# Optimization experiments

Hardware: AMD Instinct MI355X
Metric: run time of the kernel (lower is better)

The kernel has to match this reference:

```python
import jax, jax.numpy as jnp
import numpy as np

F = 256          # number of features (input_size)
H1, H2, H3 = 128, 64, 32
OUT = 1          # output_size


def setup_inputs() -> dict:
    key = jax.random.key(0)
    ks = jax.random.split(key, 10)
    B = 8192
    # Kaiming-uniform-ish small init; exact init doesn't matter for a math reference.
    def w(k, shape, fan_in):
        lim = 1.0 / np.sqrt(fan_in)
        return jax.random.uniform(k, shape, jnp.float32, -lim, lim)
    return {
        "x": jax.random.normal(ks[0], (B, F), dtype=jnp.float32),
        "W1": w(ks[1], (F, H1), 1),          # Linear(1 -> H1) per feature
        "b1": w(ks[2], (F, H1), 1),
        "W2": w(ks[3], (F, H1, H2), H1),
        "b2": w(ks[4], (F, H2), H1),
        "W3": w(ks[5], (F, H2, H3), H2),
        "b3": w(ks[6], (F, H3), H2),
        "W4": w(ks[7], (F, H3, OUT), H3),
        "b4": w(ks[8], (F, OUT), H3),
        "bias": jnp.zeros((OUT,), dtype=jnp.float32),
    }


def reference(x, W1, b1, W2, b2, W3, b3, W4, b4, bias):
    # Fused form of the per-feature FeatureNN loop (eval mode: dropout = identity).
    # Layer 1: scalar input per feature -> H1
    h = jax.nn.relu(x[:, :, None] * W1[None, :, :] + b1[None, :, :])   # [B,F,H1]
    h = jax.nn.relu(jnp.einsum('bfh,fhk->bfk', h, W2) + b2[None])      # [B,F,H2]
    h = jax.nn.relu(jnp.einsum('bfh,fhk->bfk', h, W3) + b3[None])      # [B,F,H3]
    f_out = jnp.einsum('bfh,fhk->bfk', h, W4) + b4[None]               # [B,F,OUT]
    # torch.cat(dim=1).sum(dim=1, keepdim=True): sum over features and output cols
    out = jnp.sum(f_out, axis=(1, 2), keepdims=False)[:, None] + bias[None, :]
    return out  # [B, OUT] with OUT==1
```

## Files before the change

### kernel.cpp

```cpp
#include <hip/hip_runtime.h>
#include <math.h>


#define NF   256
#define NH1  128
#define NH2  64
#define NH3  32
#define NB   8192

#define NRANK 129
#define ROW4  17
#define ROWH  136
#define TBLDW 8960

typedef float    f32x16 __attribute__((ext_vector_type(16)));
typedef unsigned u32x4  __attribute__((ext_vector_type(4)));
typedef _Float16 h16x2  __attribute__((ext_vector_type(2)));
typedef _Float16 h16x8  __attribute__((ext_vector_type(8)));

__device__ __forceinline__ unsigned pkh2(unsigned sw, unsigned sb, h16x2 xh) {
    h16x2 r = __builtin_elementwise_fma(xh, __builtin_bit_cast(h16x2, sw),
                                            __builtin_bit_cast(h16x2, sb));
    h16x2 hz = {(_Float16)0.f, (_Float16)0.f};
    return __builtin_bit_cast(unsigned, __builtin_elementwise_max(r, hz));
}

__global__ __launch_bounds__(512) void build_tables(
    const float* __restrict__ W1, const float* __restrict__ b1,
    const float* __restrict__ W2, const float* __restrict__ b2,
    const float* __restrict__ bias, float* __restrict__ out,
    unsigned* __restrict__ ws)
{
    __shared__ u32x4 SP4[NRANK * ROW4];
    __shared__ float tkey[NH1];
    __shared__ int   tidx[NH1];
    __shared__ float w1s[NH1], b1s[NH1];
    __shared__ float Pbw[8][NH2], Pbb[8][NH2], Pdw[8][NH2], Pdb[8][NH2];

    const int f = blockIdx.x;
    const int t = (int)threadIdx.x;
    _Float16* SPh = (_Float16*)SP4;

    const int gid = f * 512 + t;
    if (gid < NB) out[gid] = bias[0];

    const float* __restrict__ gw2 = W2 + (size_t)f * NH1 * NH2;
    if (t < NH1) {
        float w  = W1[f * NH1 + t];
        float bb = b1[f * NH1 + t];
        w1s[t] = w; b1s[t] = bb;
        tkey[t] = (w != 0.0f) ? (-bb / w) : INFINITY;
        tidx[t] = t;
    }
    __syncthreads();

    for (int size = 2; size <= NH1; size <<= 1) {
        for (int stride = size >> 1; stride > 0; stride >>= 1) {
            if (t < 64) {
                int pos = ((t / stride) * (stride << 1)) + (t % stride);
                int par = pos + stride;
                bool up = ((pos & size) == 0);
                float a = tkey[pos], c = tkey[par];
                int  ia = tidx[pos], ic = tidx[par];
                if ((a > c) == up) {
                    tkey[pos] = c; tkey[par] = a;
                    tidx[pos] = ic; tidx[par] = ia;
                }
            }
            __syncthreads();
        }
    }

    {
        const int k = t & 63, c = t >> 6;
        float bw = 0.0f, bbp = 0.0f, dw = 0.0f, db = 0.0f;
        #pragma unroll 4
        for (int i = 0; i < 16; ++i) {
            int j = c * 16 + i;
            float w = w1s[j], bv = b1s[j], w2v = gw2[j * NH2 + k];
            if (w < 0.0f) { bw = fmaf(w, w2v, bw); bbp = fmaf(bv, w2v, bbp); }
            else if (w == 0.0f && bv > 0.0f) { bbp = fmaf(bv, w2v, bbp); }
            int jj = tidx[c * 16 + i];
            float ww = w1s[jj], bv2 = b1s[jj], w2x = gw2[jj * NH2 + k];
            float s = (ww > 0.0f) ? 1.0f : ((ww < 0.0f) ? -1.0f : 0.0f);
            dw = fmaf(s * ww,  w2x, dw);
            db = fmaf(s * bv2, w2x, db);
        }
        Pbw[c][k] = bw; Pbb[c][k] = bbp; Pdw[c][k] = dw; Pdb[c][k] = db;
    }
    __syncthreads();
    {
        const int k = t & 63, c = t >> 6;
        float accw = 0.0f;
        float accb = b2[f * NH2 + k];
        #pragma unroll
        for (int c2 = 0; c2 < 8; ++c2) { accw += Pbw[c2][k]; accb += Pbb[c2][k]; }
        for (int c2 = 0; c2 < c; ++c2) { accw += Pdw[c2][k]; accb += Pdb[c2][k]; }
        if (c == 0) {
            SPh[k]      = (_Float16)accw;
            SPh[64 + k] = (_Float16)accb;
        }
        #pragma unroll 4
        for (int i = 0; i < 16; ++i) {
            int r = c * 16 + i;
            int j = tidx[r];
            float w = w1s[j], bv = b1s[j], w2v = gw2[j * NH2 + k];
            float s = (w > 0.0f) ? 1.0f : ((w < 0.0f) ? -1.0f : 0.0f);
            accw = fmaf(s * w,  w2v, accw);
            accb = fmaf(s * bv, w2v, accb);
            SPh[(r + 1) * ROWH + k]      = (_Float16)accw;
            SPh[(r + 1) * ROWH + 64 + k] = (_Float16)accb;
        }
    }
    __syncthreads();

    unsigned* __restrict__ wsf = ws + (size_t)f * TBLDW;
    if (t < NH1) wsf[t] = __float_as_uint(tkey[t]);
    const u32x4* src = (const u32x4*)SP4;
    u32x4* dst = (u32x4*)(wsf + NH1);
    #pragma unroll 2
    for (int i = t; i < NRANK * ROW4; i += 512) dst[i] = src[i];
}

__global__ __launch_bounds__(512, 4) void nam_main(
    const float* __restrict__ x,
    const float* __restrict__ W3, const float* __restrict__ b3,
    const float* __restrict__ W4, const float* __restrict__ b4,
    const unsigned* __restrict__ ws,
    float* __restrict__ out)
{
    __shared__ u32x4 SP4[NRANK * ROW4];
    __shared__ float tkey[NH1];

    const int f  = blockIdx.x >> 2;
    const int qt = blockIdx.x & 3;
    const int t  = (int)threadIdx.x;

    const unsigned* __restrict__ wsf = ws + (size_t)f * TBLDW;
    if (t < NH1) tkey[t] = __uint_as_float(wsf[t]);
    {
        const u32x4* src = (const u32x4*)(wsf + NH1);
        #pragma unroll 2
        for (int i = t; i < NRANK * ROW4; i += 512) SP4[i] = src[i];
    }
    __syncthreads();

    const int lane = t & 63, wv = t >> 6;
    const int n = lane & 31, q2 = lane >> 5;

    const float* __restrict__ w3g = W3 + f * NH2 * NH3;
    h16x8 A0, A1, A2, A3;
    #pragma unroll
    for (int j = 0; j < 8; ++j) {
        int kk = q2 * 8 + j;
        A0[j] = (_Float16)w3g[kk * NH3 + n];
        A1[j] = (_Float16)w3g[(kk + 16) * NH3 + n];
        A2[j] = (_Float16)w3g[(kk + 32) * NH3 + n];
        A3[j] = (_Float16)w3g[(kk + 48) * NH3 + n];
    }
    float b3r[16], w4r[16];
    #pragma unroll
    for (int reg = 0; reg < 16; ++reg) {
        int row = (reg & 3) + 8 * (reg >> 2) + 4 * q2;
        b3r[reg] = b3[f * NH3 + row];
        w4r[reg] = W4[f * NH3 + row];
    }
    const float b4f = b4[f];
    const float t63 = tkey[63], t31 = tkey[31], t95 = tkey[95];
    const float t15 = tkey[15], t47 = tkey[47], t79 = tkey[79], t111 = tkey[111];

    #pragma unroll 1
    for (int round = 0; round < 8; ++round) {
        const int base = qt * 2048 + (round * 8 + wv) * 32;
        const float xv = x[(size_t)(base + n) * NF + f];

        int r = (t63 < xv) ? 64 : 0;
        {
            float l1 = (r & 64) ? t95 : t31;
            if (l1 < xv) r += 32;
            float m0 = (r & 64) ? t79  : t15;
            float m1 = (r & 64) ? t111 : t47;
            float l2 = (r & 32) ? m1 : m0;
            if (l2 < xv) r += 16;
        }
        #pragma unroll
        for (int s = 8; s > 0; s >>= 1)
            if (tkey[r + s - 1] < xv) r += s;

        const int ro = r * ROW4;
        u32x4 SW0 = SP4[ro + q2],      SW1 = SP4[ro + 2 + q2];
        u32x4 SW2 = SP4[ro + 4 + q2],  SW3 = SP4[ro + 6 + q2];
        u32x4 SB0 = SP4[ro + 8 + q2],  SB1 = SP4[ro + 10 + q2];
        u32x4 SB2 = SP4[ro + 12 + q2], SB3 = SP4[ro + 14 + q2];

        const h16x2 xh = {(_Float16)xv, (_Float16)xv};
        u32x4 d0, d1, d2, d3;
        d0.x = pkh2(SW0.x, SB0.x, xh); d0.y = pkh2(SW0.y, SB0.y, xh);
        d0.z = pkh2(SW0.z, SB0.z, xh); d0.w = pkh2(SW0.w, SB0.w, xh);
        d1.x = pkh2(SW1.x, SB1.x, xh); d1.y = pkh2(SW1.y, SB1.y, xh);
        d1.z = pkh2(SW1.z, SB1.z, xh); d1.w = pkh2(SW1.w, SB1.w, xh);
        d2.x = pkh2(SW2.x, SB2.x, xh); d2.y = pkh2(SW2.y, SB2.y, xh);
        d2.z = pkh2(SW2.z, SB2.z, xh); d2.w = pkh2(SW2.w, SB2.w, xh);
        d3.x = pkh2(SW3.x, SB3.x, xh); d3.y = pkh2(SW3.y, SB3.y, xh);
        d3.z = pkh2(SW3.z, SB3.z, xh); d3.w = pkh2(SW3.w, SB3.w, xh);
        h16x8 B0 = __builtin_bit_cast(h16x8, d0);
        h16x8 B1 = __builtin_bit_cast(h16x8, d1);
        h16x8 B2 = __builtin_bit_cast(h16x8, d2);
        h16x8 B3 = __builtin_bit_cast(h16x8, d3);

        f32x16 acc;
        #pragma unroll
        for (int reg = 0; reg < 16; ++reg) acc[reg] = b3r[reg];
        acc = __builtin_amdgcn_mfma_f32_32x32x16_f16(A0, B0, acc, 0, 0, 0);
        acc = __builtin_amdgcn_mfma_f32_32x32x16_f16(A1, B1, acc, 0, 0, 0);
        acc = __builtin_amdgcn_mfma_f32_32x32x16_f16(A2, B2, acc, 0, 0, 0);
        acc = __builtin_amdgcn_mfma_f32_32x32x16_f16(A3, B3, acc, 0, 0, 0);

        float p = 0.0f;
        #pragma unroll
        for (int reg = 0; reg < 16; ++reg)
            p = fmaf(fmaxf(acc[reg], 0.0f), w4r[reg], p);
        p += __shfl_xor(p, 32);
        if (lane < 32) atomicAdd(&out[base + lane], p + b4f);
    }
}

extern "C" void kernel_launch(void* const* d_in, const int* in_sizes, int n_in,
                              void* d_out, int out_size, void* d_ws, size_t ws_size,
                              hipStream_t stream) {
    const float* x    = (const float*)d_in[0];
    const float* W1   = (const float*)d_in[1];
    const float* b1   = (const float*)d_in[2];
    const float* W2   = (const float*)d_in[3];
    const float* b2   = (const float*)d_in[4];
    const float* W3   = (const float*)d_in[5];
    const float* b3   = (const float*)d_in[6];
    const float* W4   = (const float*)d_in[7];
    const float* b4   = (const float*)d_in[8];
    const float* bias = (const float*)d_in[9];
    float* out   = (float*)d_out;
    unsigned* ws = (unsigned*)d_ws;

    build_tables<<<NF, 512, 0, stream>>>(W1, b1, W2, b2, bias, out, ws);
    nam_main<<<NF * 4, 512, 0, stream>>>(x, W3, b3, W4, b4, ws, out);
}
```

Measured before the change: 121.6 us.

## Replace bitonic sort with rank sort, widen table build, prefetch x in main loop

The table-building kernel swaps the barrier-heavy bitonic sort of breakpoints for a single-pass rank-counting sort. It also doubles the block to 1024 threads, so each thread handles 8 instead of 16 rows of the prefix scan. The main kernel software-pipelines the batch loop: it loads the next x value and computes its rank search while the current MFMA chain runs, and it feeds the bias vector straight in as the MFMA accumulator. The costs are more shared memory and registers, one wasted prefetch on the last round (index wraps), and 1024-thread blocks for the build.

New measurement: 121.1 us. Within noise of the previous version (-0.4%).

```diff
diff --git a/kernel.cpp b/kernel.cpp
--- a/kernel.cpp
+++ b/kernel.cpp
@@ -25,23 +25,24 @@
     return __builtin_bit_cast(unsigned, __builtin_elementwise_max(r, hz));
 }
 
-__global__ __launch_bounds__(512) void build_tables(
+__global__ __launch_bounds__(1024) void build_tables(
     const float* __restrict__ W1, const float* __restrict__ b1,
     const float* __restrict__ W2, const float* __restrict__ b2,
     const float* __restrict__ bias, float* __restrict__ out,
     unsigned* __restrict__ ws)
 {
     __shared__ u32x4 SP4[NRANK * ROW4];
-    __shared__ float tkey[NH1];
-    __shared__ int   tidx[NH1];
+    __shared__ float rkey[NH1];
+    __shared__ float skey[NH1];
+    __shared__ int   sidx[NH1];
     __shared__ float w1s[NH1], b1s[NH1];
-    __shared__ float Pbw[8][NH2], Pbb[8][NH2], Pdw[8][NH2], Pdb[8][NH2];
+    __shared__ float Pbw[16][NH2], Pbb[16][NH2], Pdw[16][NH2], Pdb[16][NH2];
 
     const int f = blockIdx.x;
     const int t = (int)threadIdx.x;
     _Float16* SPh = (_Float16*)SP4;
 
-    const int gid = f * 512 + t;
+    const int gid = f * 1024 + t;
     if (gid < NB) out[gid] = bias[0];
 
     const float* __restrict__ gw2 = W2 + (size_t)f * NH1 * NH2;
@@ -49,38 +50,32 @@
         float w  = W1[f * NH1 + t];
         float bb = b1[f * NH1 + t];
         w1s[t] = w; b1s[t] = bb;
-        tkey[t] = (w != 0.0f) ? (-bb / w) : INFINITY;
-        tidx[t] = t;
-    }
-    __syncthreads();
-
-    for (int size = 2; size <= NH1; size <<= 1) {
-        for (int stride = size >> 1; stride > 0; stride >>= 1) {
-            if (t < 64) {
-                int pos = ((t / stride) * (stride << 1)) + (t % stride);
-                int par = pos + stride;
-                bool up = ((pos & size) == 0);
-                float a = tkey[pos], c = tkey[par];
-                int  ia = tidx[pos], ic = tidx[par];
-                if ((a > c) == up) {
-                    tkey[pos] = c; tkey[par] = a;
-                    tidx[pos] = ic; tidx[par] = ia;
-                }
-            }
-            __syncthreads();
-        }
-    }
+        rkey[t] = (w != 0.0f) ? (-bb / w) : INFINITY;
+    }
+    __syncthreads();
+
+    if (t < NH1) {
+        const float my = rkey[t];
+        int rk = 0;
+        #pragma unroll 16
+        for (int i = 0; i < NH1; ++i) {
+            float ki = rkey[i];
+            rk += (ki < my || (ki == my && i < t)) ? 1 : 0;
+        }
+        skey[rk] = my; sidx[rk] = t;
+    }
+    __syncthreads();
 
     {
         const int k = t & 63, c = t >> 6;
         float bw = 0.0f, bbp = 0.0f, dw = 0.0f, db = 0.0f;
-        #pragma unroll 4
-        for (int i = 0; i < 16; ++i) {
-            int j = c * 16 + i;
+        #pragma unroll
+        for (int i = 0; i < 8; ++i) {
+            int j = c * 8 + i;
             float w = w1s[j], bv = b1s[j], w2v = gw2[j * NH2 + k];
             if (w < 0.0f) { bw = fmaf(w, w2v, bw); bbp = fmaf(bv, w2v, bbp); }
             else if (w == 0.0f && bv > 0.0f) { bbp = fmaf(bv, w2v, bbp); }
-            int jj = tidx[c * 16 + i];
+            int jj = sidx[c * 8 + i];
             float ww = w1s[jj], bv2 = b1s[jj], w2x = gw2[jj * NH2 + k];
             float s = (ww > 0.0f) ? 1.0f : ((ww < 0.0f) ? -1.0f : 0.0f);
             dw = fmaf(s * ww,  w2x, dw);
@@ -94,16 +89,16 @@
         float accw = 0.0f;
         float accb = b2[f * NH2 + k];
         #pragma unroll
-        for (int c2 = 0; c2 < 8; ++c2) { accw += Pbw[c2][k]; accb += Pbb[c2][k]; }
+        for (int c2 = 0; c2 < 16; ++c2) { accw += Pbw[c2][k]; accb += Pbb[c2][k]; }
         for (int c2 = 0; c2 < c; ++c2) { accw += Pdw[c2][k]; accb += Pdb[c2][k]; }
         if (c == 0) {
             SPh[k]      = (_Float16)accw;
             SPh[64 + k] = (_Float16)accb;
         }
-        #pragma unroll 4
-        for (int i = 0; i < 16; ++i) {
-            int r = c * 16 + i;
-            int j = tidx[r];
+        #pragma unroll
+        for (int i = 0; i < 8; ++i) {
+            int r = c * 8 + i;
+            int j = sidx[r];
             float w = w1s[j], bv = b1s[j], w2v = gw2[j * NH2 + k];
             float s = (w > 0.0f) ? 1.0f : ((w < 0.0f) ? -1.0f : 0.0f);
             accw = fmaf(s * w,  w2v, accw);
@@ -115,11 +110,10 @@
     __syncthreads();
 
     unsigned* __restrict__ wsf = ws + (size_t)f * TBLDW;
-    if (t < NH1) wsf[t] = __float_as_uint(tkey[t]);
+    if (t < NH1) wsf[t] = __float_as_uint(skey[t]);
     const u32x4* src = (const u32x4*)SP4;
     u32x4* dst = (u32x4*)(wsf + NH1);
-    #pragma unroll 2
-    for (int i = t; i < NRANK * ROW4; i += 512) dst[i] = src[i];
+    for (int i = t; i < NRANK * ROW4; i += 1024) dst[i] = src[i];
 }
 
 __global__ __launch_bounds__(512, 4) void nam_main(
@@ -158,34 +152,44 @@
         A2[j] = (_Float16)w3g[(kk + 32) * NH3 + n];
         A3[j] = (_Float16)w3g[(kk + 48) * NH3 + n];
     }
-    float b3r[16], w4r[16];
+    f32x16 bacc;
+    float w4r[16];
     #pragma unroll
     for (int reg = 0; reg < 16; ++reg) {
         int row = (reg & 3) + 8 * (reg >> 2) + 4 * q2;
-        b3r[reg] = b3[f * NH3 + row];
-        w4r[reg] = W4[f * NH3 + row];
+        bacc[reg] = b3[f * NH3 + row];
+        w4r[reg]  = W4[f * NH3 + row];
     }
     const float b4f = b4[f];
     const float t63 = tkey[63], t31 = tkey[31], t95 = tkey[95];
     const float t15 = tkey[15], t47 = tkey[47], t79 = tkey[79], t111 = tkey[111];
 
+    auto rankof = [&](float q) -> int {
+        int rr = (t63 < q) ? 64 : 0;
+        {
+            float l1 = (rr & 64) ? t95 : t31;
+            if (l1 < q) rr += 32;
+            float m0 = (rr & 64) ? t79  : t15;
+            float m1 = (rr & 64) ? t111 : t47;
+            float l2 = (rr & 32) ? m1 : m0;
+            if (l2 < q) rr += 16;
+        }
+        #pragma unroll
+        for (int s = 8; s > 0; s >>= 1)
+            if (tkey[rr + s - 1] < q) rr += s;
+        return rr;
+    };
+
+    const int base0 = qt * 2048 + wv * 32;
+    float xv = x[(size_t)(base0 + n) * NF + f];
+    int r = rankof(xv);
+
     #pragma unroll 1
     for (int round = 0; round < 8; ++round) {
-        const int base = qt * 2048 + (round * 8 + wv) * 32;
-        const float xv = x[(size_t)(base + n) * NF + f];
-
-        int r = (t63 < xv) ? 64 : 0;
-        {
-            float l1 = (r & 64) ? t95 : t31;
-            if (l1 < xv) r += 32;
-            float m0 = (r & 64) ? t79  : t15;
-            float m1 = (r & 64) ? t111 : t47;
-            float l2 = (r & 32) ? m1 : m0;
-            if (l2 < xv) r += 16;
-        }
-        #pragma unroll
-        for (int s = 8; s > 0; s >>= 1)
-            if (tkey[r + s - 1] < xv) r += s;
+        const int base = base0 + round * 256;
+
+        const int nidx = (base + 256 + n) & (NB - 1);
+        const float xnext = x[(size_t)nidx * NF + f];
 
         const int ro = r * ROW4;
         u32x4 SW0 = SP4[ro + q2],      SW1 = SP4[ro + 2 + q2];
@@ -208,13 +212,12 @@
         h16x8 B2 = __builtin_bit_cast(h16x8, d2);
         h16x8 B3 = __builtin_bit_cast(h16x8, d3);
 
-        f32x16 acc;
-        #pragma unroll
-        for (int reg = 0; reg < 16; ++reg) acc[reg] = b3r[reg];
-        acc = __builtin_amdgcn_mfma_f32_32x32x16_f16(A0, B0, acc, 0, 0, 0);
+        f32x16 acc = __builtin_amdgcn_mfma_f32_32x32x16_f16(A0, B0, bacc, 0, 0, 0);
         acc = __builtin_amdgcn_mfma_f32_32x32x16_f16(A1, B1, acc, 0, 0, 0);
         acc = __builtin_amdgcn_mfma_f32_32x32x16_f16(A2, B2, acc, 0, 0, 0);
         acc = __builtin_amdgcn_mfma_f32_32x32x16_f16(A3, B3, acc, 0, 0, 0);
+
+        const int rnext = rankof(xnext);
 
         float p = 0.0f;
         #pragma unroll
@@ -222,6 +225,8 @@
             p = fmaf(fmaxf(acc[reg], 0.0f), w4r[reg], p);
         p += __shfl_xor(p, 32);
         if (lane < 32) atomicAdd(&out[base + lane], p + b4f);
+
+        xv = xnext; r = rnext;
     }
 }
 
@@ -241,6 +246,6 @@
     float* out   = (float*)d_out;
     unsigned* ws = (unsigned*)d_ws;
 
-    build_tables<<<NF, 512, 0, stream>>>(W1, b1, W2, b2, bias, out, ws);
+    build_tables<<<NF, 1024, 0, stream>>>(W1, b1, W2, b2, bias, out, ws);
     nam_main<<<NF * 4, 512, 0, stream>>>(x, W3, b3, W4, b4, ws, out);
 }
```
